# Kernel tuning notes

Hardware: AMD Instinct MI355X
Metric: run time of the kernel (lower is better)

The kernel has to match this reference:

```python
import jax, jax.numpy as jnp
import numpy as np

N, F, E, C = 50000, 128, 800000, 10

def setup_inputs() -> dict:
    key = jax.random.key(0)
    ks = jax.random.split(key, 16)
    s = 1.0 / np.sqrt(F)
    def u(k, shape):
        return jax.random.uniform(k, shape, jnp.float32, -s, s)
    inp = {
        "x": jax.random.normal(ks[0], (N, F), jnp.float32),
        "edge_index": jax.random.randint(ks[1], (2, E), 0, N),
    }
    for i, p in enumerate(["1", "2"]):
        b = 2 + i * 5
        inp["W" + p] = u(ks[b], (F, F))          # EvolveGCNO initial_weight
        inp["wih" + p] = u(ks[b + 1], (3 * F, F))  # GRU input weights (r,z,n)
        inp["whh" + p] = u(ks[b + 2], (3 * F, F))  # GRU hidden weights
        inp["bih" + p] = u(ks[b + 3], (3 * F,))
        inp["bhh" + p] = u(ks[b + 4], (3 * F,))
    inp["lin_w"] = u(ks[12], (C, F))
    inp["lin_b"] = u(ks[13], (C,))
    return inp

def gru_step(x, h, wih, whh, bih, bhh):
    # torch.nn.GRU single step; gate order r, z, n
    gi = x @ wih.T + bih
    gh = h @ whh.T + bhh
    ir, iz, inn = jnp.split(gi, 3, axis=-1)
    hr, hz, hn = jnp.split(gh, 3, axis=-1)
    r = jax.nn.sigmoid(ir + hr)
    z = jax.nn.sigmoid(iz + hz)
    n = jnp.tanh(inn + r * hn)
    return (1.0 - z) * n + z * h

def gcn_conv(W, x, src, dst):
    # GCNConv_Fixed_W: gcn_norm with self-loops, then aggregate (x @ W)
    n = x.shape[0]
    loop = jnp.arange(n)
    s = jnp.concatenate([src, loop])
    d = jnp.concatenate([dst, loop])
    deg = jax.ops.segment_sum(jnp.ones(s.shape[0], x.dtype), d, num_segments=n)
    dinv = jnp.where(deg > 0, jax.lax.rsqrt(deg), 0.0)
    norm = dinv[s] * dinv[d]                 # [E+N]
    xw = x @ W                               # [N, F]
    return jax.ops.segment_sum(norm[:, None] * xw[s], d, num_segments=n)

def evolve_gcno(x, src, dst, W0, wih, whh, bih, bhh):
    # weight evolved by GRU with input = hidden = current weight
    W = gru_step(W0, W0, wih, whh, bih, bhh)
    return gcn_conv(W, x, src, dst)

def reference(x, edge_index, W1, wih1, whh1, bih1, bhh1,
              W2, wih2, whh2, bih2, bhh2, lin_w, lin_b):
    src, dst = edge_index[0], edge_index[1]
    h = jax.nn.relu(evolve_gcno(x, src, dst, W1, wih1, whh1, bih1, bhh1))
    # dropout is identity in eval mode
    h = jax.nn.relu(evolve_gcno(h, src, dst, W2, wih2, whh2, bih2, bhh2))
    logits = h @ lin_w.T + lin_b
    return jax.nn.log_softmax(logits, axis=1)
```

## Files before the change

### kernel.cpp

```cpp
#include <hip/hip_runtime.h>
#include <cstddef>
#include <cstdint>

#define F 128
#define C_OUT 10
#define SB 256

typedef short bf16x8 __attribute__((ext_vector_type(8)));
typedef float f32x4  __attribute__((ext_vector_type(4)));
typedef float f32x2  __attribute__((ext_vector_type(2)));

__device__ __forceinline__ unsigned short bf16_rne(float f) {
  unsigned u = __float_as_uint(f);
  return (unsigned short)((u + 0x7FFFu + ((u >> 16) & 1u)) >> 16);
}

__global__ void gru_evolve2_k(const float* __restrict__ W01, const float* __restrict__ wih1,
                              const float* __restrict__ whh1, const float* __restrict__ bih1,
                              const float* __restrict__ bhh1,
                              const float* __restrict__ W02, const float* __restrict__ wih2,
                              const float* __restrict__ whh2, const float* __restrict__ bih2,
                              const float* __restrict__ bhh2,
                              unsigned short* __restrict__ Bhi1, unsigned short* __restrict__ Bhi2,
                              int* __restrict__ counts, int n) {
  if ((int)blockIdx.x >= 128) {
    int i = ((int)blockIdx.x - 128) * SB + threadIdx.x;
    if (i < n) counts[i] = 0;
    return;
  }
  int t = blockIdx.x * 256 + threadIdx.x;
  int layer = t >> 14;
  int tt = t & 16383;
  const float* W0  = layer ? W02  : W01;
  const float* wih = layer ? wih2 : wih1;
  const float* whh = layer ? whh2 : whh1;
  const float* bih = layer ? bih2 : bih1;
  const float* bhh = layer ? bhh2 : bhh1;
  unsigned short* Bhi = layer ? Bhi2 : Bhi1;
  int i = tt >> 7, j = tt & 127;
  const float4* w0r = (const float4*)(W0 + (size_t)i * F);
  float gi[3], gh[3];
#pragma unroll
  for (int g = 0; g < 3; ++g) {
    const float4* wr = (const float4*)(wih + (size_t)(g * F + j) * F);
    const float4* hr = (const float4*)(whh + (size_t)(g * F + j) * F);
    float si = 0.f, sh = 0.f;
    for (int k = 0; k < F / 4; ++k) {
      float4 a = w0r[k];
      float4 b = wr[k];
      float4 c = hr[k];
      si += a.x * b.x + a.y * b.y + a.z * b.z + a.w * b.w;
      sh += a.x * c.x + a.y * c.y + a.z * c.z + a.w * c.w;
    }
    gi[g] = si + bih[g * F + j];
    gh[g] = sh + bhh[g * F + j];
  }
  float r = 1.0f / (1.0f + expf(-(gi[0] + gh[0])));
  float z = 1.0f / (1.0f + expf(-(gi[1] + gh[1])));
  float nn = tanhf(gi[2] + r * gh[2]);
  float val = (1.0f - z) * nn + z * W0[(size_t)i * F + j];

  int kstep = i >> 5, kl = i & 31;
  int lane = (kl >> 3) * 16 + (j & 15);
  int tile = j >> 4;
  int idx = ((kstep * 8 + tile) * 64 + lane) * 8 + (kl & 7);
  Bhi[idx] = bf16_rne(val);
}

__global__ void count_rank_k(const int* __restrict__ dst, int* __restrict__ counts,
                             int* __restrict__ rank, int E) {
  int e = blockIdx.x * blockDim.x + threadIdx.x;
  if (e < E) rank[e] = atomicAdd(&counts[dst[e]], 1);
}

__global__ void scan_local_k(const int* __restrict__ counts, int* __restrict__ incl,
                             int* __restrict__ blocksum, int n) {
  __shared__ int sh[SB];
  int gid = blockIdx.x * SB + threadIdx.x;
  int v = (gid < n) ? counts[gid] : 0;
  sh[threadIdx.x] = v;
  __syncthreads();
  for (int off = 1; off < SB; off <<= 1) {
    int t = 0;
    if ((int)threadIdx.x >= off) t = sh[threadIdx.x - off];
    __syncthreads();
    if ((int)threadIdx.x >= off) sh[threadIdx.x] += t;
    __syncthreads();
  }
  if (gid < n) incl[gid] = sh[threadIdx.x];
  if (threadIdx.x == SB - 1) blocksum[blockIdx.x] = sh[SB - 1];
}

__global__ void scan_finish_k(const int* __restrict__ counts, const int* __restrict__ incl,
                              const int* __restrict__ blocksum, int* __restrict__ rowptr,
                              float* __restrict__ dinv, int n, int nb) {
  __shared__ int sh[SB];
  __shared__ int orig[SB];
  int v = ((int)threadIdx.x < nb) ? blocksum[threadIdx.x] : 0;
  sh[threadIdx.x] = v;
  orig[threadIdx.x] = v;
  __syncthreads();
  for (int off = 1; off < SB; off <<= 1) {
    int t = 0;
    if ((int)threadIdx.x >= off) t = sh[threadIdx.x - off];
    __syncthreads();
    if ((int)threadIdx.x >= off) sh[threadIdx.x] += t;
    __syncthreads();
  }
  int myoff = sh[blockIdx.x] - orig[blockIdx.x];
  int gid = blockIdx.x * SB + threadIdx.x;
  if (gid >= n) return;
  int c = counts[gid];
  int inc = myoff + incl[gid];
  rowptr[gid] = inc - c;
  dinv[gid] = rsqrtf((float)c + 1.0f);
  if (gid == n - 1) rowptr[n] = inc;
}

__device__ __forceinline__ void fill_body(int bid, const int* __restrict__ src,
                                          const int* __restrict__ dst,
                                          const int* __restrict__ rank,
                                          const int* __restrict__ rowptr,
                                          int* __restrict__ csr_src, int E) {
  int e = bid * 256 + (int)threadIdx.x;
  if (e < E) {
    int d = dst[e];
    csr_src[rowptr[d] + rank[e]] = src[e] << 7;
  }
}

__device__ __forceinline__ void gemm_body(int bid, const float* __restrict__ X,
                                          const unsigned short* __restrict__ Bhi,
                                          const float* __restrict__ dinv,
                                          unsigned* __restrict__ Y, int nrows) {
  int wid = bid * 4 + ((int)threadIdx.x >> 6);
  int lane = threadIdx.x & 63;
  int ng = (nrows + 15) >> 4;
  if (wid >= ng) return;
  int g = __builtin_amdgcn_readfirstlane(wid);
  int q = lane >> 4, m = lane & 15;
  int rowA = g * 16 + m;
  if (rowA >= nrows) rowA = nrows - 1;

  f32x4 acc[8];
#pragma unroll
  for (int t = 0; t < 8; ++t) { acc[t].x = 0.f; acc[t].y = 0.f; acc[t].z = 0.f; acc[t].w = 0.f; }

#pragma unroll
  for (int s = 0; s < 4; ++s) {
    const float* xp = X + (size_t)rowA * F + s * 32 + q * 8;
    float4 xa = *(const float4*)xp;
    float4 xb = *(const float4*)(xp + 4);
    float xv[8] = {xa.x, xa.y, xa.z, xa.w, xb.x, xb.y, xb.z, xb.w};
    bf16x8 xh;
#pragma unroll
    for (int j = 0; j < 8; ++j) xh[j] = (short)bf16_rne(xv[j]);
#pragma unroll
    for (int t = 0; t < 8; ++t) {
      size_t boff = ((size_t)(s * 8 + t) * 64 + lane) * 8;
      bf16x8 wh = *(const bf16x8*)(Bhi + boff);
      acc[t] = __builtin_amdgcn_mfma_f32_16x16x32_bf16(wh, xh, acc[t], 0, 0, 0);
    }
  }

  int row = g * 16 + m;
  if (row < nrows) {
    float dd = dinv[row];
    unsigned* yr = Y + (size_t)row * 32 + q;
#pragma unroll
    for (int t = 0; t < 8; ++t) {
      int p = __builtin_amdgcn_cvt_pk_fp8_f32(dd * acc[t].x, dd * acc[t].y, 0, false);
      p = __builtin_amdgcn_cvt_pk_fp8_f32(dd * acc[t].z, dd * acc[t].w, p, true);
      yr[t * 4] = (unsigned)p;
    }
  }
}

__global__ void gemm_mfma_k(const float* __restrict__ X, const unsigned short* __restrict__ Bhi,
                            const float* __restrict__ dinv, unsigned* __restrict__ Y,
                            int nrows) {
  gemm_body(blockIdx.x, X, Bhi, dinv, Y, nrows);
}

__global__ void fill_gemm_k(const float* __restrict__ X, const unsigned short* __restrict__ Bhi,
                            const float* __restrict__ dinv, unsigned* __restrict__ Y,
                            int nrows, int ngemm,
                            const int* __restrict__ src, const int* __restrict__ dst,
                            const int* __restrict__ rank, const int* __restrict__ rowptr,
                            int* __restrict__ csr_src, int E) {
  if ((int)blockIdx.x < ngemm)
    gemm_body(blockIdx.x, X, Bhi, dinv, Y, nrows);
  else
    fill_body((int)blockIdx.x - ngemm, src, dst, rank, rowptr, csr_src, E);
}

template <bool FUSE_LOGITS>
__global__ __launch_bounds__(256, 4)
void agg_fp8_k(const int* __restrict__ rowptr, const int* __restrict__ csr_src,
               const float* __restrict__ dinv, const unsigned* __restrict__ xwp,
               float* __restrict__ hout,
               const float* __restrict__ lw, const float* __restrict__ lb,
               float* __restrict__ outp, int n) {
  int wave = (int)((blockIdx.x * blockDim.x + threadIdx.x) >> 6);
  int lane = threadIdx.x & 63;
  if (wave >= n) return;
  int node = __builtin_amdgcn_readfirstlane(wave);
  int half = lane >> 5, hm = lane & 31;
  const char* __restrict__ cb = (const char*)xwp;
  unsigned loff = (unsigned)(hm << 2);

  unsigned uself = *(const unsigned*)(cb + ((((unsigned)node) << 7) | loff));

  int b = rowptr[node], e = rowptr[node + 1];
  float dd = dinv[node];
  if (half) uself = 0u;

  f32x2 acc0 = {0.f, 0.f}, acc1 = {0.f, 0.f};
  f32x2 bcc0 = {0.f, 0.f}, bcc1 = {0.f, 0.f};

#define DEC(U, A, B)                                           \
  do {                                                         \
    (A) += __builtin_amdgcn_cvt_pk_f32_fp8((int)(U), false);   \
    (B) += __builtin_amdgcn_cvt_pk_f32_fp8((int)(U), true);    \
  } while (0)

  DEC(uself, acc0, acc1);

  const int* __restrict__ cp = csr_src + half;
  int i = b;
  for (; i + 32 <= e; i += 32) {
    int sv[16];
#pragma unroll
    for (int k = 0; k < 16; ++k) sv[k] = cp[i + 2 * k];
    unsigned uv[16];
#pragma unroll
    for (int k = 0; k < 16; ++k)
      uv[k] = *(const unsigned*)(cb + (((unsigned)sv[k]) | loff));
#pragma unroll
    for (int k = 0; k < 16; ++k) {
      if (k & 1) DEC(uv[k], bcc0, bcc1); else DEC(uv[k], acc0, acc1);
    }
  }
  if (i < e) {
    int em1 = e - 1;
    int ih = i + half;
    int sv[16];
#pragma unroll
    for (int k = 0; k < 16; ++k) {
      int off = ih + 2 * k;
      sv[k] = csr_src[off > em1 ? em1 : off];
    }
    unsigned uv[16];
#pragma unroll
    for (int k = 0; k < 16; ++k)
      uv[k] = *(const unsigned*)(cb + (((unsigned)sv[k]) | loff));
#pragma unroll
    for (int k = 0; k < 16; ++k) {
      unsigned u = (ih + 2 * k < e) ? uv[k] : 0u;
      if (k & 1) DEC(u, bcc0, bcc1); else DEC(u, acc0, acc1);
    }
  }
#undef DEC
  acc0 += bcc0;
  acc1 += bcc1;

  acc0.x += __shfl_xor(acc0.x, 32);
  acc0.y += __shfl_xor(acc0.y, 32);
  acc1.x += __shfl_xor(acc1.x, 32);
  acc1.y += __shfl_xor(acc1.y, 32);

  float h0 = fmaxf(dd * acc0.x, 0.f);
  float h1 = fmaxf(dd * acc0.y, 0.f);
  float h2 = fmaxf(dd * acc1.x, 0.f);
  float h3 = fmaxf(dd * acc1.y, 0.f);

  if (!FUSE_LOGITS) {
    if (half == 0) {
      *(float4*)(hout + (size_t)node * F + hm * 4) = make_float4(h0, h1, h2, h3);
    }
  } else {
    float acc[C_OUT];
#pragma unroll
    for (int c = 0; c < C_OUT; ++c) {
      float4 w = *(const float4*)(lw + (size_t)c * F + hm * 4);
      float v = h0 * w.x + h1 * w.y + h2 * w.z + h3 * w.w;
      v += __shfl_xor(v, 1); v += __shfl_xor(v, 2);
      v += __shfl_xor(v, 4); v += __shfl_xor(v, 8);
      v += __shfl_xor(v, 16);
      acc[c] = v + lb[c];
    }
    float mx = acc[0];
#pragma unroll
    for (int c = 1; c < C_OUT; ++c) mx = fmaxf(mx, acc[c]);
    float s = 0.f;
#pragma unroll
    for (int c = 0; c < C_OUT; ++c) s += expf(acc[c] - mx);
    float lse = mx + logf(s);
#pragma unroll
    for (int c = 0; c < C_OUT; ++c)
      if (lane == c) outp[(size_t)node * C_OUT + c] = acc[c] - lse;
  }
}

extern "C" void kernel_launch(void* const* d_in, const int* in_sizes, int n_in,
                              void* d_out, int out_size, void* d_ws, size_t ws_size,
                              hipStream_t stream) {
  const float* x    = (const float*)d_in[0];
  const int*   ei   = (const int*)d_in[1];
  const float* W1   = (const float*)d_in[2];
  const float* wih1 = (const float*)d_in[3];
  const float* whh1 = (const float*)d_in[4];
  const float* bih1 = (const float*)d_in[5];
  const float* bhh1 = (const float*)d_in[6];
  const float* W2   = (const float*)d_in[7];
  const float* wih2 = (const float*)d_in[8];
  const float* whh2 = (const float*)d_in[9];
  const float* bih2 = (const float*)d_in[10];
  const float* bhh2 = (const float*)d_in[11];
  const float* lw   = (const float*)d_in[12];
  const float* lb   = (const float*)d_in[13];
  float* out = (float*)d_out;

  int N = in_sizes[0] / F;
  int E = in_sizes[1] / 2;
  const int* src = ei;
  const int* dst = ei + E;
  int nb = (N + SB - 1) / SB;
  int ng = (N + 15) / 16;
  int ngemm = (ng + 3) / 4;
  int nfill = (E + 255) / 256;
  int nagg = (N + 3) / 4;

  float* ws = (float*)d_ws;
  unsigned* bufA = (unsigned*)ws;
  float* bufB = (float*)(bufA + (size_t)N * 32);
  float* dinv = bufB + (size_t)N * F;
  unsigned short* Bhi1 = (unsigned short*)(dinv + N);
  unsigned short* Bhi2 = Bhi1 + F * F;
  int* counts = (int*)(Bhi2 + F * F);
  int* rowptr = counts + N;
  int* rank   = rowptr + N + 1;
  int* incl   = rank + E;
  int* blocksum = incl + N;
  int* csr_src = blocksum + 256;

  gru_evolve2_k<<<128 + nb, 256, 0, stream>>>(W1, wih1, whh1, bih1, bhh1,
                                              W2, wih2, whh2, bih2, bhh2,
                                              Bhi1, Bhi2, counts, N);

  count_rank_k<<<(E + 255) / 256, 256, 0, stream>>>(dst, counts, rank, E);
  scan_local_k<<<nb, SB, 0, stream>>>(counts, incl, blocksum, N);
  scan_finish_k<<<nb, SB, 0, stream>>>(counts, incl, blocksum, rowptr, dinv, N, nb);

  fill_gemm_k<<<ngemm + nfill, 256, 0, stream>>>(x, Bhi1, dinv, bufA, N, ngemm,
                                                 src, dst, rank, rowptr, csr_src, E);
  agg_fp8_k<false><<<nagg, 256, 0, stream>>>(rowptr, csr_src, dinv, bufA, bufB,
                                             nullptr, nullptr, nullptr, N);

  gemm_mfma_k<<<ngemm, 256, 0, stream>>>(bufB, Bhi2, dinv, bufA, N);
  agg_fp8_k<true><<<nagg, 256, 0, stream>>>(rowptr, csr_src, dinv, bufA, nullptr,
                                            lw, lb, out, N);
}
```

Before: 263.3 us.

## Split FP8 feature table into two column planes and aggregate each plane separately

The GEMM now writes its FP8 output as two 64-column planes (64 bytes per row each), and every aggregation runs as two passes, one per plane. The intent is to halve the gather footprint per pass so it fits better in cache (about 3.2MB per plane) and raises L2 hit rates on random neighbour gathers. The logits are split into partial dot products stored in a temporary buffer, with log-softmax finished in the second pass. In exchange, rowptr and csr_src are read twice, there are extra kernel launches, and nontemporal stores are used for the hidden output.

```diff
diff --git a/kernel.cpp b/kernel.cpp
--- a/kernel.cpp
+++ b/kernel.cpp
@@ -13,6 +13,11 @@
 __device__ __forceinline__ unsigned short bf16_rne(float f) {
   unsigned u = __float_as_uint(f);
   return (unsigned short)((u + 0x7FFFu + ((u >> 16) & 1u)) >> 16);
+}
+
+__device__ __forceinline__ void dec2(unsigned u, f32x2& A, f32x2& B) {
+  A += __builtin_amdgcn_cvt_pk_f32_fp8((int)u, false);
+  B += __builtin_amdgcn_cvt_pk_f32_fp8((int)u, true);
 }
 
 __global__ void gru_evolve2_k(const float* __restrict__ W01, const float* __restrict__ wih1,
@@ -125,7 +130,7 @@
   int e = bid * 256 + (int)threadIdx.x;
   if (e < E) {
     int d = dst[e];
-    csr_src[rowptr[d] + rank[e]] = src[e] << 7;
+    csr_src[rowptr[d] + rank[e]] = src[e] << 6;
   }
 }
 
@@ -166,12 +171,13 @@
   int row = g * 16 + m;
   if (row < nrows) {
     float dd = dinv[row];
-    unsigned* yr = Y + (size_t)row * 32 + q;
+    size_t pstr = (size_t)nrows * 16;
+    unsigned* y0 = Y + (size_t)row * 16 + q;
 #pragma unroll
     for (int t = 0; t < 8; ++t) {
       int p = __builtin_amdgcn_cvt_pk_fp8_f32(dd * acc[t].x, dd * acc[t].y, 0, false);
       p = __builtin_amdgcn_cvt_pk_fp8_f32(dd * acc[t].z, dd * acc[t].w, p, true);
-      yr[t * 4] = (unsigned)p;
+      *(y0 + (t >= 4 ? pstr : 0) + (t & 3) * 4) = (unsigned)p;
     }
   }
 }
@@ -194,111 +200,125 @@
     fill_body((int)blockIdx.x - ngemm, src, dst, rank, rowptr, csr_src, E);
 }
 
-template <bool FUSE_LOGITS>
-__global__ __launch_bounds__(256, 4)
-void agg_fp8_k(const int* __restrict__ rowptr, const int* __restrict__ csr_src,
-               const float* __restrict__ dinv, const unsigned* __restrict__ xwp,
-               float* __restrict__ hout,
-               const float* __restrict__ lw, const float* __restrict__ lb,
-               float* __restrict__ outp, int n) {
+template <int OUT_MODE>
+__global__ void agg_half_k(const int* __restrict__ rowptr, const int* __restrict__ csr_src,
+                           const float* __restrict__ dinv, const unsigned* __restrict__ plane,
+                           float* __restrict__ hout, float* __restrict__ plog,
+                           const float* __restrict__ lw, const float* __restrict__ lb,
+                           float* __restrict__ outp, int n, int pofs) {
   int wave = (int)((blockIdx.x * blockDim.x + threadIdx.x) >> 6);
   int lane = threadIdx.x & 63;
   if (wave >= n) return;
   int node = __builtin_amdgcn_readfirstlane(wave);
-  int half = lane >> 5, hm = lane & 31;
-  const char* __restrict__ cb = (const char*)xwp;
+  int slot = lane >> 4, hm = lane & 15;
   unsigned loff = (unsigned)(hm << 2);
-
-  unsigned uself = *(const unsigned*)(cb + ((((unsigned)node) << 7) | loff));
+  const char* __restrict__ cb = (const char*)plane;
+
+  unsigned uself = *(const unsigned*)(cb + ((((unsigned)node) << 6) | loff));
 
   int b = rowptr[node], e = rowptr[node + 1];
   float dd = dinv[node];
-  if (half) uself = 0u;
-
-  f32x2 acc0 = {0.f, 0.f}, acc1 = {0.f, 0.f};
-  f32x2 bcc0 = {0.f, 0.f}, bcc1 = {0.f, 0.f};
-
-#define DEC(U, A, B)                                           \
-  do {                                                         \
-    (A) += __builtin_amdgcn_cvt_pk_f32_fp8((int)(U), false);   \
-    (B) += __builtin_amdgcn_cvt_pk_f32_fp8((int)(U), true);    \
-  } while (0)
-
-  DEC(uself, acc0, acc1);
-
-  const int* __restrict__ cp = csr_src + half;
+  if (slot) uself = 0u;
+
+  f32x2 a0 = {0.f, 0.f}, a1 = {0.f, 0.f};
+  f32x2 b0 = {0.f, 0.f}, b1 = {0.f, 0.f};
+  dec2(uself, a0, a1);
+
+  const int* __restrict__ cp = csr_src + slot;
   int i = b;
-  for (; i + 32 <= e; i += 32) {
-    int sv[16];
-#pragma unroll
-    for (int k = 0; k < 16; ++k) sv[k] = cp[i + 2 * k];
-    unsigned uv[16];
-#pragma unroll
-    for (int k = 0; k < 16; ++k)
-      uv[k] = *(const unsigned*)(cb + (((unsigned)sv[k]) | loff));
-#pragma unroll
-    for (int k = 0; k < 16; ++k) {
-      if (k & 1) DEC(uv[k], bcc0, bcc1); else DEC(uv[k], acc0, acc1);
-    }
+  for (; i + 16 <= e; i += 16) {
+    int s0 = cp[i], s1 = cp[i + 4], s2 = cp[i + 8], s3 = cp[i + 12];
+    unsigned u0 = *(const unsigned*)(cb + (((unsigned)s0) | loff));
+    unsigned u1 = *(const unsigned*)(cb + (((unsigned)s1) | loff));
+    unsigned u2 = *(const unsigned*)(cb + (((unsigned)s2) | loff));
+    unsigned u3 = *(const unsigned*)(cb + (((unsigned)s3) | loff));
+    dec2(u0, a0, a1);
+    dec2(u1, b0, b1);
+    dec2(u2, a0, a1);
+    dec2(u3, b0, b1);
   }
   if (i < e) {
     int em1 = e - 1;
-    int ih = i + half;
-    int sv[16];
-#pragma unroll
-    for (int k = 0; k < 16; ++k) {
-      int off = ih + 2 * k;
-      sv[k] = csr_src[off > em1 ? em1 : off];
-    }
-    unsigned uv[16];
-#pragma unroll
-    for (int k = 0; k < 16; ++k)
-      uv[k] = *(const unsigned*)(cb + (((unsigned)sv[k]) | loff));
-#pragma unroll
-    for (int k = 0; k < 16; ++k) {
-      unsigned u = (ih + 2 * k < e) ? uv[k] : 0u;
-      if (k & 1) DEC(u, bcc0, bcc1); else DEC(u, acc0, acc1);
-    }
-  }
-#undef DEC
-  acc0 += bcc0;
-  acc1 += bcc1;
-
-  acc0.x += __shfl_xor(acc0.x, 32);
-  acc0.y += __shfl_xor(acc0.y, 32);
-  acc1.x += __shfl_xor(acc1.x, 32);
-  acc1.y += __shfl_xor(acc1.y, 32);
-
-  float h0 = fmaxf(dd * acc0.x, 0.f);
-  float h1 = fmaxf(dd * acc0.y, 0.f);
-  float h2 = fmaxf(dd * acc1.x, 0.f);
-  float h3 = fmaxf(dd * acc1.y, 0.f);
-
-  if (!FUSE_LOGITS) {
-    if (half == 0) {
-      *(float4*)(hout + (size_t)node * F + hm * 4) = make_float4(h0, h1, h2, h3);
+    int ih = i + slot;
+    int o0 = ih,     o1 = ih + 4,  o2 = ih + 8,  o3 = ih + 12;
+    int c0 = o0 > em1 ? em1 : o0, c1 = o1 > em1 ? em1 : o1;
+    int c2 = o2 > em1 ? em1 : o2, c3 = o3 > em1 ? em1 : o3;
+    int s0 = csr_src[c0], s1 = csr_src[c1], s2 = csr_src[c2], s3 = csr_src[c3];
+    unsigned u0 = *(const unsigned*)(cb + (((unsigned)s0) | loff));
+    unsigned u1 = *(const unsigned*)(cb + (((unsigned)s1) | loff));
+    unsigned u2 = *(const unsigned*)(cb + (((unsigned)s2) | loff));
+    unsigned u3 = *(const unsigned*)(cb + (((unsigned)s3) | loff));
+    if (o0 >= e) u0 = 0u;
+    if (o1 >= e) u1 = 0u;
+    if (o2 >= e) u2 = 0u;
+    if (o3 >= e) u3 = 0u;
+    dec2(u0, a0, a1);
+    dec2(u1, b0, b1);
+    dec2(u2, a0, a1);
+    dec2(u3, b0, b1);
+  }
+  a0 += b0;
+  a1 += b1;
+
+  a0.x += __shfl_xor(a0.x, 16); a0.y += __shfl_xor(a0.y, 16);
+  a1.x += __shfl_xor(a1.x, 16); a1.y += __shfl_xor(a1.y, 16);
+  a0.x += __shfl_xor(a0.x, 32); a0.y += __shfl_xor(a0.y, 32);
+  a1.x += __shfl_xor(a1.x, 32); a1.y += __shfl_xor(a1.y, 32);
+
+  float h0 = fmaxf(dd * a0.x, 0.f);
+  float h1 = fmaxf(dd * a0.y, 0.f);
+  float h2 = fmaxf(dd * a1.x, 0.f);
+  float h3 = fmaxf(dd * a1.y, 0.f);
+
+  if (OUT_MODE == 0) {
+    if (slot == 0) {
+      f32x4 hv = {h0, h1, h2, h3};
+      __builtin_nontemporal_store(hv, (f32x4*)(hout + (size_t)node * F + pofs + hm * 4));
     }
   } else {
-    float acc[C_OUT];
-#pragma unroll
-    for (int c = 0; c < C_OUT; ++c) {
-      float4 w = *(const float4*)(lw + (size_t)c * F + hm * 4);
-      float v = h0 * w.x + h1 * w.y + h2 * w.z + h3 * w.w;
-      v += __shfl_xor(v, 1); v += __shfl_xor(v, 2);
-      v += __shfl_xor(v, 4); v += __shfl_xor(v, 8);
-      v += __shfl_xor(v, 16);
-      acc[c] = v + lb[c];
-    }
-    float mx = acc[0];
-#pragma unroll
-    for (int c = 1; c < C_OUT; ++c) mx = fmaxf(mx, acc[c]);
-    float s = 0.f;
-#pragma unroll
-    for (int c = 0; c < C_OUT; ++c) s += expf(acc[c] - mx);
-    float lse = mx + logf(s);
-#pragma unroll
-    for (int c = 0; c < C_OUT; ++c)
-      if (lane == c) outp[(size_t)node * C_OUT + c] = acc[c] - lse;
+    int cc2 = (slot < 2) ? slot + 8 : slot;
+#define PDOT(CC, DST)                                                      \
+    do {                                                                   \
+      float4 w = *(const float4*)(lw + (size_t)(CC) * F + pofs + hm * 4);  \
+      float v_ = h0 * w.x + h1 * w.y + h2 * w.z + h3 * w.w;                \
+      v_ += __shfl_xor(v_, 1); v_ += __shfl_xor(v_, 2);                    \
+      v_ += __shfl_xor(v_, 4); v_ += __shfl_xor(v_, 8);                    \
+      DST = v_;                                                            \
+    } while (0)
+    float v0, v1, v2;
+    PDOT(slot, v0);
+    PDOT(slot + 4, v1);
+    PDOT(cc2, v2);
+#undef PDOT
+    if (OUT_MODE == 1) {
+      if (hm == 0) {
+        plog[(size_t)node * C_OUT + slot] = v0;
+        plog[(size_t)node * C_OUT + slot + 4] = v1;
+        if (slot < 2) plog[(size_t)node * C_OUT + slot + 8] = v2;
+      }
+    } else {
+      v0 += plog[(size_t)node * C_OUT + slot] + lb[slot];
+      v1 += plog[(size_t)node * C_OUT + slot + 4] + lb[slot + 4];
+      v2 += plog[(size_t)node * C_OUT + cc2] + lb[cc2];
+      bool has2 = (slot < 2);
+      float ml = fmaxf(v0, v1);
+      if (has2) ml = fmaxf(ml, v2);
+      if (hm != 0) ml = -3.0e38f;
+      ml = fmaxf(ml, __shfl_xor(ml, 16));
+      ml = fmaxf(ml, __shfl_xor(ml, 32));
+      float se = 0.f;
+      if (hm == 0) {
+        se = expf(v0 - ml) + expf(v1 - ml) + (has2 ? expf(v2 - ml) : 0.f);
+      }
+      se += __shfl_xor(se, 16);
+      se += __shfl_xor(se, 32);
+      float lse = ml + logf(se);
+      if (hm == 0) {
+        outp[(size_t)node * C_OUT + slot] = v0 - lse;
+        outp[(size_t)node * C_OUT + slot + 4] = v1 - lse;
+        if (has2) outp[(size_t)node * C_OUT + slot + 8] = v2 - lse;
+      }
+    }
   }
 }
 
@@ -343,6 +363,10 @@
   int* incl   = rank + E;
   int* blocksum = incl + N;
   int* csr_src = blocksum + 256;
+  float* plog = (float*)(csr_src + E);
+
+  unsigned* plane0 = bufA;
+  unsigned* plane1 = bufA + (size_t)N * 16;
 
   gru_evolve2_k<<<128 + nb, 256, 0, stream>>>(W1, wih1, whh1, bih1, bhh1,
                                               W2, wih2, whh2, bih2, bhh2,
@@ -354,10 +378,14 @@
 
   fill_gemm_k<<<ngemm + nfill, 256, 0, stream>>>(x, Bhi1, dinv, bufA, N, ngemm,
                                                  src, dst, rank, rowptr, csr_src, E);
-  agg_fp8_k<false><<<nagg, 256, 0, stream>>>(rowptr, csr_src, dinv, bufA, bufB,
-                                             nullptr, nullptr, nullptr, N);
+  agg_half_k<0><<<nagg, 256, 0, stream>>>(rowptr, csr_src, dinv, plane0, bufB,
+                                          nullptr, nullptr, nullptr, nullptr, N, 0);
+  agg_half_k<0><<<nagg, 256, 0, stream>>>(rowptr, csr_src, dinv, plane1, bufB,
+                                          nullptr, nullptr, nullptr, nullptr, N, 64);
 
   gemm_mfma_k<<<ngemm, 256, 0, stream>>>(bufB, Bhi2, dinv, bufA, N);
-  agg_fp8_k<true><<<nagg, 256, 0, stream>>>(rowptr, csr_src, dinv, bufA, nullptr,
-                                            lw, lb, out, N);
-}
+  agg_half_k<1><<<nagg, 256, 0, stream>>>(rowptr, csr_src, dinv, plane0, nullptr,
+                                          plog, lw, nullptr, nullptr, N, 0);
+  agg_half_k<2><<<nagg, 256, 0, stream>>>(rowptr, csr_src, dinv, plane1, nullptr,
+                                          plog, lw, lb, out, N, 64);
+}
```

After: 274.8 us. 1.04x slower.
